# Kernel optimization log

Measured on AMD Instinct MI355X. Metric: run time of the kernel, lower is better.

## Reference

```python
import jax, jax.numpy as jnp
import numpy as np

M, N, K, C, G = 16384, 131072, 16, 128, 8
EPS_BN = 1e-5


def _bn(x, g, b):
    # inference-mode BatchNorm1d (running_mean=0, running_var=1)
    return x * (g / jnp.sqrt(1.0 + EPS_BN)) + b


def setup_inputs() -> dict:
    key = jax.random.key(0)
    ks = jax.random.split(key, 16)
    f32 = jnp.float32
    s = 0.05
    return {
        "query_feat": jax.random.normal(ks[0], (M, C), f32),
        "context_feat": jax.random.normal(ks[1], (N, C), f32),
        "query_coord": jax.random.normal(ks[2], (M, 3), f32),
        "context_coord": jax.random.normal(ks[3], (N, 3), f32),
        "Wq": jax.random.normal(ks[4], (C, C), f32) * s,
        "bq": jnp.zeros((C,), f32),
        "gq": jnp.ones((C,), f32),
        "betaq": jnp.zeros((C,), f32),
        "Wk": jax.random.normal(ks[5], (C, C), f32) * s,
        "bk": jnp.zeros((C,), f32),
        "gk": jnp.ones((C,), f32),
        "betak": jnp.zeros((C,), f32),
        "Wv": jax.random.normal(ks[6], (C, C), f32) * s,
        "bv": jnp.zeros((C,), f32),
        "Wp1": jax.random.normal(ks[7], (3, C), f32) * s,
        "bp1": jnp.zeros((C,), f32),
        "gp1": jnp.ones((C,), f32),
        "betap1": jnp.zeros((C,), f32),
        "Wp2": jax.random.normal(ks[8], (C, C), f32) * s,
        "bp2": jnp.zeros((C,), f32),
        "Ww1": jax.random.normal(ks[9], (C, G), f32) * s,
        "bw1": jnp.zeros((G,), f32),
        "gw1": jnp.ones((G,), f32),
        "betaw1": jnp.zeros((G,), f32),
        "Ww2": jax.random.normal(ks[10], (G, G), f32) * s,
        "bw2": jnp.zeros((G,), f32),
        "knn_indexes": jax.random.randint(ks[11], (M, K), 0, N, dtype=jnp.int32),
    }


def reference(query_feat, context_feat, query_coord, context_coord,
              Wq, bq, gq, betaq, Wk, bk, gk, betak, Wv, bv,
              Wp1, bp1, gp1, betap1, Wp2, bp2,
              Ww1, bw1, gw1, betaw1, Ww2, bw2, knn_indexes):
    q = jax.nn.relu(_bn(query_feat @ Wq + bq, gq, betaq))              # (M, C)
    k = jax.nn.relu(_bn(context_feat @ Wk + bk, gk, betak))            # (N, C)
    v = context_feat @ Wv + bv                                         # (N, C)

    mask = knn_indexes >= 0                                            # (M, K); -1 = padded neighbor
    idx = jnp.where(mask, knn_indexes, 0)
    mf = mask[..., None].astype(q.dtype)                               # (M, K, 1)

    key_g = k[idx] * mf                                                # (M, K, C) gather (zero row for -1)
    val_g = v[idx] * mf                                                # (M, K, C)
    pos = (context_coord[idx] - query_coord[:, None, :]) * mf          # (M, K, 3) relative position

    # positional-encoding bias branch (pe_bias=True, pe_multiplier=False)
    peb = jax.nn.relu(_bn(pos @ Wp1 + bp1, gp1, betap1)) @ Wp2 + bp2   # (M, K, C)
    rel = key_g - q[:, None, :] + peb                                  # (M, K, C)
    val_g = val_g + peb

    # grouped vector attention weights
    w = jax.nn.relu(_bn(rel @ Ww1 + bw1, gw1, betaw1)) @ Ww2 + bw2     # (M, K, G)
    w = jax.nn.softmax(w, axis=1) * mf                                 # softmax over neighbors, mask padded

    m_, k_ = idx.shape
    c_ = q.shape[-1]
    g_ = w.shape[-1]
    out = jnp.einsum('mkgi,mkg->mgi', val_g.reshape(m_, k_, g_, c_ // g_), w)
    return out.reshape(m_, c_)
```

## Files before the change

kernel.cpp:

```cpp
#include <hip/hip_runtime.h>

#define C 128
#define G 8
#define KNN 16
#define QB 4
#define EPS 1e-5f

typedef unsigned short u16;
typedef __attribute__((ext_vector_type(8))) short short8;
typedef __attribute__((ext_vector_type(4))) float float4v;

union frag_u { short8 v; u16 u[8]; unsigned d[4]; };

__device__ inline u16 f2bf(float f) {
    unsigned u = __builtin_bit_cast(unsigned, f);
    unsigned r = (u + 0x7fffu + ((u >> 16) & 1u)) >> 16;
    return (u16)r;
}
__device__ inline float bf2f(u16 h) {
    unsigned u = ((unsigned)h) << 16;
    return __builtin_bit_cast(float, u);
}
__device__ inline unsigned pk2(float lo, float hi) {
    unsigned r;
    asm("v_cvt_pk_bf16_f32 %0, %1, %2" : "=v"(r) : "v"(lo), "v"(hi));
    return r;
}
__device__ inline u16 f2bf1(float f) { return (u16)pk2(f, f); }
__device__ inline float bflo(unsigned v) { return __builtin_bit_cast(float, v << 16); }
__device__ inline float bfhi(unsigned v) { return __builtin_bit_cast(float, v & 0xffff0000u); }

__global__ __launch_bounds__(256) void prep_w(
    const float* __restrict__ Wk, const float* __restrict__ Wv,
    const float* __restrict__ Wq, const float* __restrict__ Wp2,
    const float* __restrict__ Ww1, const float* __restrict__ bp2,
    u16* __restrict__ dst, float* __restrict__ cw1)
{
    __shared__ float w1s[C * G];
    const int b = blockIdx.x, t = threadIdx.x;
    if (b < 16) {
        const int mi = b >> 2, qt = b & 3;
        const float* W = mi == 0 ? Wk : mi == 1 ? Wv : mi == 2 ? Wq : Wp2;
        u16* d = dst + mi * 16384;
        for (int e = qt * 4096 + t; e < (qt + 1) * 4096; e += 256) {
            const int k = e >> 7, n = e & 127;
            const int cb = n >> 4, lan = n & 15;
            const int kk = k >> 5, quad = (k >> 3) & 3, j = k & 7;
            d[(((cb * 4 + kk) * 4 + quad) * 16 + lan) * 8 + j] = f2bf(W[e]);
        }
    } else if (b == 16) {
        u16* d = dst + 4 * 16384;
        for (int e = t; e < 4096; e += 256) {
            const int j = e & 7, lan = (e >> 3) & 15;
            const int quad = (e >> 7) & 3, kk = e >> 9;
            const int k = kk * 32 + quad * 8 + j;
            d[e] = lan < 8 ? f2bf(Ww1[k * G + lan]) : (u16)0;
        }
    } else {
        u16* d = dst + 4 * 16384 + 4096;
        for (int e = t; e < 4096; e += 256) d[e] = 0;
        for (int e = t; e < C * G; e += 256) w1s[e] = Ww1[e];
        __syncthreads();
#pragma unroll
        for (int it = 0; it < 4; it++) {
            const int k = it * 32 + (t >> 3), g = t & 7;
            const float4* Wr = (const float4*)(Wp2 + k * C);
            float a = 0.f;
#pragma unroll 8
            for (int i4 = 0; i4 < 32; i4++) {
                const float4 wv = Wr[i4];
                a = fmaf(wv.x, w1s[(i4 * 4 + 0) * G + g], a);
                a = fmaf(wv.y, w1s[(i4 * 4 + 1) * G + g], a);
                a = fmaf(wv.z, w1s[(i4 * 4 + 2) * G + g], a);
                a = fmaf(wv.w, w1s[(i4 * 4 + 3) * G + g], a);
            }
            const int kk = k >> 5, quad = (k >> 3) & 3, j = k & 7;
            d[((kk * 4 + quad) * 16 + g) * 8 + j] = f2bf(a);
        }
        if (t < G) {
            float a = 0.f;
#pragma unroll 8
            for (int i = 0; i < C; i++) a = fmaf(bp2[i], w1s[i * G + t], a);
            cw1[t] = a;
        }
    }
}

__global__ __launch_bounds__(256) void proj_all(
    const float* __restrict__ Xc, const float* __restrict__ Xq,
    const u16* __restrict__ PWk, const float* __restrict__ bk,
    const float* __restrict__ gk, const float* __restrict__ betak,
    const u16* __restrict__ PWv, const float* __restrict__ bv,
    const u16* __restrict__ PWq, const float* __restrict__ bq,
    const float* __restrict__ gq, const float* __restrict__ betaq,
    const u16* __restrict__ PWw1b,
    u16* __restrict__ vout, u16* __restrict__ Kp, u16* __restrict__ Qp,
    int nkv)
{
    __shared__ u16 Xs[64 * 136];
    const int t = threadIdx.x;
    const int w = t >> 6, l = t & 63;
    const int quad = l >> 4, lan = l & 15;
    const bool isq = (int)blockIdx.x >= nkv;
    const long long row0 = (long long)(isq ? blockIdx.x - nkv : blockIdx.x) * 64;
    const float* X = isq ? Xq : Xc;

    {
        const float4* Xv = (const float4*)(X + row0 * C);
#pragma unroll
        for (int i = 0; i < 8; i++) {
            const int e = t + 256 * i;
            const int r = e >> 5, c4 = e & 31;
            const float4 f = Xv[e];
            uint2 p;
            p.x = pk2(f.x, f.y);
            p.y = pk2(f.z, f.w);
            *(uint2*)(&Xs[r * 136 + c4 * 4]) = p;
        }
    }
    __syncthreads();

    if (!isq) {
        unsigned vp[2][4][2];
        {
            short8 Bf[2][4];
#pragma unroll
            for (int ct = 0; ct < 2; ct++) {
                const int cb = w * 2 + ct;
#pragma unroll
                for (int kk = 0; kk < 4; kk++)
                    Bf[ct][kk] = *(const short8*)(PWv + (((cb * 4 + kk) * 4 + quad) * 16 + lan) * 8);
            }
            const float b0v = bv[w * 32 + lan], b1v = bv[w * 32 + 16 + lan];
            float4v acc[2][4];
#pragma unroll
            for (int rt = 0; rt < 4; rt++) {
                acc[0][rt] = (float4v)b0v;
                acc[1][rt] = (float4v)b1v;
            }
#pragma unroll
            for (int rt = 0; rt < 4; rt++)
#pragma unroll
                for (int kk = 0; kk < 4; kk++) {
                    const short8 A = *(const short8*)(&Xs[(rt * 16 + lan) * 136 + kk * 32 + quad * 8]);
#pragma unroll
                    for (int ct = 0; ct < 2; ct++)
                        acc[ct][rt] = __builtin_amdgcn_mfma_f32_16x16x32_bf16(
                            A, Bf[ct][kk], acc[ct][rt], 0, 0, 0);
                }
#pragma unroll
            for (int ct = 0; ct < 2; ct++)
#pragma unroll
                for (int rt = 0; rt < 4; rt++)
#pragma unroll
                    for (int h = 0; h < 2; h++)
                        vp[ct][rt][h] = pk2(acc[ct][rt][2 * h], acc[ct][rt][2 * h + 1]);
        }
        float4v acck[2][4];
        {
            short8 Bf[2][4];
#pragma unroll
            for (int ct = 0; ct < 2; ct++) {
                const int cb = w * 2 + ct;
#pragma unroll
                for (int kk = 0; kk < 4; kk++)
                    Bf[ct][kk] = *(const short8*)(PWk + (((cb * 4 + kk) * 4 + quad) * 16 + lan) * 8);
            }
            const float b0k = bk[w * 32 + lan], b1k = bk[w * 32 + 16 + lan];
#pragma unroll
            for (int rt = 0; rt < 4; rt++) {
                acck[0][rt] = (float4v)b0k;
                acck[1][rt] = (float4v)b1k;
            }
#pragma unroll
            for (int rt = 0; rt < 4; rt++)
#pragma unroll
                for (int kk = 0; kk < 4; kk++) {
                    const short8 A = *(const short8*)(&Xs[(rt * 16 + lan) * 136 + kk * 32 + quad * 8]);
#pragma unroll
                    for (int ct = 0; ct < 2; ct++)
                        acck[ct][rt] = __builtin_amdgcn_mfma_f32_16x16x32_bf16(
                            A, Bf[ct][kk], acck[ct][rt], 0, 0, 0);
                }
        }
        __syncthreads();

#pragma unroll
        for (int ct = 0; ct < 2; ct++) {
            const int cg = w * 32 + ct * 16 + lan;
            const float sc = gk[cg] * rsqrtf(1.f + EPS);
            const float sh = betak[cg];
#pragma unroll
            for (int rt = 0; rt < 4; rt++)
#pragma unroll
                for (int reg = 0; reg < 4; reg++) {
                    float y = fmaf(acck[ct][rt][reg], sc, sh);
                    y = y > 0.f ? y : 0.f;
                    Xs[(rt * 16 + quad * 4 + reg) * 136 + cg] = f2bf1(y);
                }
        }
        __syncthreads();

        {
            short8 Bw[4];
#pragma unroll
            for (int kk = 0; kk < 4; kk++)
                Bw[kk] = *(const short8*)(PWw1b + ((kk * 4 + quad) * 16 + lan) * 8);
            float4v ka = (float4v)0.f;
#pragma unroll
            for (int kk = 0; kk < 4; kk++) {
                const short8 A = *(const short8*)(&Xs[(w * 16 + lan) * 136 + kk * 32 + quad * 8]);
                ka = __builtin_amdgcn_mfma_f32_16x16x32_bf16(A, Bw[kk], ka, 0, 0, 0);
            }
            if (lan < G) {
#pragma unroll
                for (int reg = 0; reg < 4; reg++)
                    Kp[(row0 + w * 16 + quad * 4 + reg) * G + lan] = f2bf1(ka[reg]);
            }
        }
        __syncthreads();

#pragma unroll
        for (int ct = 0; ct < 2; ct++) {
            const int cg = w * 32 + ct * 16 + lan;
#pragma unroll
            for (int rt = 0; rt < 4; rt++)
#pragma unroll
                for (int h = 0; h < 2; h++) {
                    Xs[(rt * 16 + quad * 4 + 2 * h) * 136 + cg]     = (u16)(vp[ct][rt][h] & 0xffffu);
                    Xs[(rt * 16 + quad * 4 + 2 * h + 1) * 136 + cg] = (u16)(vp[ct][rt][h] >> 16);
                }
        }
        __syncthreads();
#pragma unroll
        for (int i = 0; i < 4; i++) {
            const int e = t + 256 * i;
            const int r = e >> 4, cc = (e & 15) * 8;
            *(short8*)(vout + (row0 + r) * C + cc) = *(const short8*)(&Xs[r * 136 + cc]);
        }
    } else {
        float4v acc[2][4];
        {
            short8 Bf[2][4];
#pragma unroll
            for (int ct = 0; ct < 2; ct++) {
                const int cb = w * 2 + ct;
#pragma unroll
                for (int kk = 0; kk < 4; kk++)
                    Bf[ct][kk] = *(const short8*)(PWq + (((cb * 4 + kk) * 4 + quad) * 16 + lan) * 8);
            }
            const float b0q = bq[w * 32 + lan], b1q = bq[w * 32 + 16 + lan];
#pragma unroll
            for (int rt = 0; rt < 4; rt++) {
                acc[0][rt] = (float4v)b0q;
                acc[1][rt] = (float4v)b1q;
            }
#pragma unroll
            for (int rt = 0; rt < 4; rt++)
#pragma unroll
                for (int kk = 0; kk < 4; kk++) {
                    const short8 A = *(const short8*)(&Xs[(rt * 16 + lan) * 136 + kk * 32 + quad * 8]);
#pragma unroll
                    for (int ct = 0; ct < 2; ct++)
                        acc[ct][rt] = __builtin_amdgcn_mfma_f32_16x16x32_bf16(
                            A, Bf[ct][kk], acc[ct][rt], 0, 0, 0);
                }
        }
        __syncthreads();
#pragma unroll
        for (int ct = 0; ct < 2; ct++) {
            const int cg = w * 32 + ct * 16 + lan;
            const float sc = gq[cg] * rsqrtf(1.f + EPS);
            const float sh = betaq[cg];
#pragma unroll
            for (int rt = 0; rt < 4; rt++)
#pragma unroll
                for (int reg = 0; reg < 4; reg++) {
                    float y = fmaf(acc[ct][rt][reg], sc, sh);
                    y = y > 0.f ? y : 0.f;
                    Xs[(rt * 16 + quad * 4 + reg) * 136 + cg] = f2bf1(y);
                }
        }
        __syncthreads();
        {
            short8 Bw[4];
#pragma unroll
            for (int kk = 0; kk < 4; kk++)
                Bw[kk] = *(const short8*)(PWw1b + ((kk * 4 + quad) * 16 + lan) * 8);
            float4v qa = (float4v)0.f;
#pragma unroll
            for (int kk = 0; kk < 4; kk++) {
                const short8 A = *(const short8*)(&Xs[(w * 16 + lan) * 136 + kk * 32 + quad * 8]);
                qa = __builtin_amdgcn_mfma_f32_16x16x32_bf16(A, Bw[kk], qa, 0, 0, 0);
            }
            if (lan < G) {
#pragma unroll
                for (int reg = 0; reg < 4; reg++)
                    Qp[(row0 + w * 16 + quad * 4 + reg) * G + lan] = f2bf1(qa[reg]);
            }
        }
    }
}

__global__ __launch_bounds__(256) void attn6(
    const u16* __restrict__ vbuf, const u16* __restrict__ Kp,
    const u16* __restrict__ Qp,
    const float* __restrict__ qcoord, const float* __restrict__ ccoord,
    const float* __restrict__ Wp1, const float* __restrict__ bp1,
    const float* __restrict__ gp1, const float* __restrict__ betap1,
    const u16* __restrict__ PWp2, const float* __restrict__ bp2,
    const u16* __restrict__ PWp2pb, const float* __restrict__ cw1,
    const float* __restrict__ bw1,
    const float* __restrict__ gw1, const float* __restrict__ betaw1,
    const float* __restrict__ Ww2, const float* __restrict__ bw2,
    const int* __restrict__ knn, float* __restrict__ out)
{
    __shared__ u16    fA[64 * 136];
    __shared__ u16    kgs[64 * G];
    __shared__ float  qps[QB * G];
    __shared__ float  pebp[64 * G];
    __shared__ float  cw1s[G];
    __shared__ float  ww2s[G * G];
    __shared__ float4 ps4[64];
    __shared__ int    idxs[64];
    __shared__ float  wl[QB * 16 * G];

    const int t = threadIdx.x;
    const int w = t >> 6, l = t & 63;
    const int quad = l >> 4, lan = l & 15;
    const int m0 = blockIdx.x * QB;
    const int rsub = t >> 4;
    const int c8 = (t & 15) * 8;

    float mfr[4];
    frag_u vg[4];
#pragma unroll
    for (int p = 0; p < 4; p++) {
        const int ii = knn[m0 * KNN + p * 16 + rsub];
        mfr[p] = ii >= 0 ? 1.f : 0.f;
        const size_t i0 = ii >= 0 ? ii : 0;
        vg[p].v = *(const short8*)(vbuf + i0 * C + c8);
    }
    if (t < 64) {
        const int q = t >> 4;
        const int ii = knn[m0 * KNN + t];
        const float mf = ii >= 0 ? 1.f : 0.f;
        const int i0 = ii >= 0 ? ii : 0;
        idxs[t] = ii;
        float4 p4;
        p4.x = (ccoord[i0 * 3 + 0] - qcoord[(m0 + q) * 3 + 0]) * mf;
        p4.y = (ccoord[i0 * 3 + 1] - qcoord[(m0 + q) * 3 + 1]) * mf;
        p4.z = (ccoord[i0 * 3 + 2] - qcoord[(m0 + q) * 3 + 2]) * mf;
        p4.w = 0.f;
        ps4[t] = p4;
        *(short8*)(&kgs[t * G]) = *(const short8*)(Kp + (size_t)i0 * G);
    } else if (t < 64 + QB) {
        const int p = t - 64;
        frag_u qv;
        qv.v = *(const short8*)(Qp + (size_t)(m0 + p) * G);
#pragma unroll
        for (int j = 0; j < G; j++) qps[p * G + j] = bf2f(qv.u[j]);
    } else if (t < 68 + G) {
        cw1s[t - 68] = cw1[t - 68];
    } else if (t < 76 + G * G) {
        ww2s[t - 76] = Ww2[t - 76];
    }
    __syncthreads();

    {
        const float rsq = rsqrtf(1.f + EPS);
        const float4 gA = *(const float4*)(&gp1[c8]);
        const float4 gB = *(const float4*)(&gp1[c8 + 4]);
        const float4 bA = *(const float4*)(&bp1[c8]);
        const float4 bB = *(const float4*)(&bp1[c8 + 4]);
        const float4 eA = *(const float4*)(&betap1[c8]);
        const float4 eB = *(const float4*)(&betap1[c8 + 4]);
        const float4 xA = *(const float4*)(&Wp1[c8]);
        const float4 xB = *(const float4*)(&Wp1[c8 + 4]);
        const float4 yA = *(const float4*)(&Wp1[C + c8]);
        const float4 yB = *(const float4*)(&Wp1[C + c8 + 4]);
        const float4 zA = *(const float4*)(&Wp1[2 * C + c8]);
        const float4 zB = *(const float4*)(&Wp1[2 * C + c8 + 4]);
        const float gs[8] = {gA.x, gA.y, gA.z, gA.w, gB.x, gB.y, gB.z, gB.w};
        const float bs[8] = {bA.x, bA.y, bA.z, bA.w, bB.x, bB.y, bB.z, bB.w};
        const float es[8] = {eA.x, eA.y, eA.z, eA.w, eB.x, eB.y, eB.z, eB.w};
        const float xs[8] = {xA.x, xA.y, xA.z, xA.w, xB.x, xB.y, xB.z, xB.w};
        const float ys[8] = {yA.x, yA.y, yA.z, yA.w, yB.x, yB.y, yB.z, yB.w};
        const float zs[8] = {zA.x, zA.y, zA.z, zA.w, zB.x, zB.y, zB.z, zB.w};
        float w0f[8], w1f[8], w2f[8], bbf[8];
#pragma unroll
        for (int i2 = 0; i2 < 8; i2++) {
            const float sc = gs[i2] * rsq;
            w0f[i2] = xs[i2] * sc;
            w1f[i2] = ys[i2] * sc;
            w2f[i2] = zs[i2] * sc;
            bbf[i2] = fmaf(bs[i2], sc, es[i2]);
        }
#pragma unroll
        for (int rr = 0; rr < 4; rr++) {
            const int r = rsub * 4 + rr;
            const float4 p4 = ps4[r];
            frag_u o;
#pragma unroll
            for (int dd = 0; dd < 4; dd++) {
                const int ca = 2 * dd, cb2 = 2 * dd + 1;
                float ya = fmaf(p4.x, w0f[ca],
                           fmaf(p4.y, w1f[ca], fmaf(p4.z, w2f[ca], bbf[ca])));
                float yb = fmaf(p4.x, w0f[cb2],
                           fmaf(p4.y, w1f[cb2], fmaf(p4.z, w2f[cb2], bbf[cb2])));
                ya = ya > 0.f ? ya : 0.f;
                yb = yb > 0.f ? yb : 0.f;
                o.d[dd] = pk2(ya, yb);
            }
            *(short8*)(&fA[r * 136 + c8]) = o.v;
        }
    }
    __syncthreads();

    float4v acc[2][4];
    float4v pp = (float4v)0.f;
    {
        short8 Bf[2][4];
#pragma unroll
        for (int ct = 0; ct < 2; ct++) {
            const int cb = w * 2 + ct;
#pragma unroll
            for (int kk = 0; kk < 4; kk++)
                Bf[ct][kk] = *(const short8*)(PWp2 + (((cb * 4 + kk) * 4 + quad) * 16 + lan) * 8);
        }
        const float b0 = bp2[w * 32 + lan], b1 = bp2[w * 32 + 16 + lan];
#pragma unroll
        for (int q = 0; q < 4; q++) {
            acc[0][q] = (float4v)b0;
            acc[1][q] = (float4v)b1;
        }
#pragma unroll
        for (int q = 0; q < 4; q++)
#pragma unroll
            for (int kk = 0; kk < 4; kk++) {
                const short8 A = *(const short8*)(&fA[(q * 16 + lan) * 136 + kk * 32 + quad * 8]);
#pragma unroll
                for (int ct = 0; ct < 2; ct++)
                    acc[ct][q] = __builtin_amdgcn_mfma_f32_16x16x32_bf16(
                        A, Bf[ct][kk], acc[ct][q], 0, 0, 0);
            }
#pragma unroll
        for (int kk = 0; kk < 4; kk++) {
            const short8 Bp = *(const short8*)(PWp2pb + ((kk * 4 + quad) * 16 + lan) * 8);
            const short8 A = *(const short8*)(&fA[(w * 16 + lan) * 136 + kk * 32 + quad * 8]);
            pp = __builtin_amdgcn_mfma_f32_16x16x32_bf16(A, Bp, pp, 0, 0, 0);
        }
    }
    __syncthreads();

    {
#pragma unroll
        for (int ct = 0; ct < 2; ct++)
#pragma unroll
            for (int q = 0; q < 4; q++)
#pragma unroll
                for (int reg = 0; reg < 4; reg++)
                    fA[(q * 16 + quad * 4 + reg) * 136 + w * 32 + ct * 16 + lan] =
                        f2bf1(acc[ct][q][reg]);
        if (lan < G) {
#pragma unroll
            for (int reg = 0; reg < 4; reg++)
                pebp[(w * 16 + quad * 4 + reg) * G + lan] = pp[reg];
        }
    }
    __syncthreads();

    {
#pragma unroll
        for (int p = 0; p < 4; p++) {
            const int r = p * 16 + rsub;
            const float mf = mfr[p];
            frag_u peb, o;
            peb.v = *(const short8*)(&fA[r * 136 + c8]);
#pragma unroll
            for (int dd = 0; dd < 4; dd++) {
                const unsigned pv = peb.d[dd], vv = vg[p].d[dd];
                o.d[dd] = pk2(fmaf(bflo(vv), mf, bflo(pv)),
                              fmaf(bfhi(vv), mf, bfhi(pv)));
            }
            *(short8*)(&fA[r * 136 + c8]) = o.v;
        }
    }
    {
        const int j = l & 15;
        const int r = (w << 4) + j;
        const float mf = idxs[r] >= 0 ? 1.f : 0.f;
        const int g0 = 2 * quad, g1 = g0 + 1;
        const float L0 = bf2f(kgs[r * G + g0]) * mf - qps[w * G + g0]
                       + pebp[r * G + g0] + cw1s[g0] + bw1[g0];
        const float L1 = bf2f(kgs[r * G + g1]) * mf - qps[w * G + g1]
                       + pebp[r * G + g1] + cw1s[g1] + bw1[g1];
        const float y0 = L0 * (gw1[g0] * rsqrtf(1.f + EPS)) + betaw1[g0];
        const float y1 = L1 * (gw1[g1] * rsqrtf(1.f + EPS)) + betaw1[g1];
        wl[w * 128 + j * 8 + g0] = y0 > 0.f ? y0 : 0.f;
        wl[w * 128 + j * 8 + g1] = y1 > 0.f ? y1 : 0.f;
    }
    __syncthreads();

    {
        const int j = l & 15;
        const int g0 = 2 * quad, g1 = g0 + 1;
        float hw_[8];
#pragma unroll
        for (int g = 0; g < 8; g++) hw_[g] = wl[w * 128 + j * 8 + g];
        float a0 = bw2[g0], a1 = bw2[g1];
#pragma unroll
        for (int g = 0; g < 8; g++) {
            a0 = fmaf(hw_[g], ww2s[g * 8 + g0], a0);
            a1 = fmaf(hw_[g], ww2s[g * 8 + g1], a1);
        }
        float mx0 = a0, mx1 = a1;
#pragma unroll
        for (int off = 1; off < 16; off <<= 1) {
            mx0 = fmaxf(mx0, __shfl_xor(mx0, off));
            mx1 = fmaxf(mx1, __shfl_xor(mx1, off));
        }
        const float e0 = __expf(a0 - mx0), e1 = __expf(a1 - mx1);
        float s0 = e0, s1 = e1;
#pragma unroll
        for (int off = 1; off < 16; off <<= 1) {
            s0 += __shfl_xor(s0, off);
            s1 += __shfl_xor(s1, off);
        }
        const float mf = idxs[(w << 4) + j] >= 0 ? 1.f : 0.f;
        wl[w * 128 + j * 8 + g0] = e0 * (1.f / s0) * mf;
        wl[w * 128 + j * 8 + g1] = e1 * (1.f / s1) * mf;
    }
    __syncthreads();

    {
        const int q = t >> 6;
        const int pc = t & 63;
        const int c0 = 2 * pc;
        const int g = pc >> 3;
        float s0 = 0.f, s1 = 0.f;
#pragma unroll
        for (int j = 0; j < KNN; j++) {
            const unsigned v = *(const unsigned*)(&fA[(q * 16 + j) * 136 + c0]);
            const float wv = wl[q * 128 + j * 8 + g];
            s0 = fmaf(bflo(v), wv, s0);
            s1 = fmaf(bfhi(v), wv, s1);
        }
        *(float2*)(&out[(size_t)(m0 + q) * C + c0]) = make_float2(s0, s1);
    }
}

extern "C" void kernel_launch(void* const* d_in, const int* in_sizes, int n_in,
                              void* d_out, int out_size, void* d_ws, size_t ws_size,
                              hipStream_t stream)
{
    const float* query_feat    = (const float*)d_in[0];
    const float* context_feat  = (const float*)d_in[1];
    const float* query_coord   = (const float*)d_in[2];
    const float* context_coord = (const float*)d_in[3];
    const float* Wq    = (const float*)d_in[4];
    const float* bq    = (const float*)d_in[5];
    const float* gq    = (const float*)d_in[6];
    const float* betaq = (const float*)d_in[7];
    const float* Wk    = (const float*)d_in[8];
    const float* bk    = (const float*)d_in[9];
    const float* gk    = (const float*)d_in[10];
    const float* betak = (const float*)d_in[11];
    const float* Wv    = (const float*)d_in[12];
    const float* bv    = (const float*)d_in[13];
    const float* Wp1   = (const float*)d_in[14];
    const float* bp1   = (const float*)d_in[15];
    const float* gp1   = (const float*)d_in[16];
    const float* betap1= (const float*)d_in[17];
    const float* Wp2   = (const float*)d_in[18];
    const float* bp2   = (const float*)d_in[19];
    const float* Ww1   = (const float*)d_in[20];
    const float* bw1   = (const float*)d_in[21];
    const float* gw1   = (const float*)d_in[22];
    const float* betaw1= (const float*)d_in[23];
    const float* Ww2   = (const float*)d_in[24];
    const float* bw2   = (const float*)d_in[25];
    const int*   knn   = (const int*)d_in[26];

    const int M = in_sizes[0] / C;
    const int N = in_sizes[1] / C;

    u16* vb = (u16*)d_ws;
    u16* Kp = vb + (size_t)N * C;
    u16* Qp = Kp + (size_t)N * G;
    u16* pw = Qp + (size_t)M * G;
    u16* pWk    = pw;
    u16* pWv    = pw + 16384;
    u16* pWq    = pw + 2 * 16384;
    u16* pWp2   = pw + 3 * 16384;
    u16* pWw1b  = pw + 4 * 16384;
    u16* pWp2pb = pw + 4 * 16384 + 4096;
    float* cw1  = (float*)(pw + 4 * 16384 + 2 * 4096);

    prep_w<<<18, 256, 0, stream>>>(Wk, Wv, Wq, Wp2, Ww1, bp2, pw, cw1);
    proj_all<<<N / 64 + M / 64, 256, 0, stream>>>(
        context_feat, query_feat,
        pWk, bk, gk, betak, pWv, bv,
        pWq, bq, gq, betaq, pWw1b,
        vb, Kp, Qp, N / 64);
    attn6<<<M / QB, 256, 0, stream>>>(vb, Kp, Qp, query_coord, context_coord,
                                      Wp1, bp1, gp1, betap1, pWp2, bp2,
                                      pWp2pb, cw1, bw1, gw1, betaw1, Ww2, bw2,
                                      knn, (float*)d_out);
}
```

Measured before the change: 206.4 us.

## Process two query groups per block and prefetch next group's value gathers

The attention kernel now handles two groups of four queries per block in a loop, halving the grid size. All knn indices, coordinates, K/Q slices for both groups are loaded up front, and the value-row gather for the next group is issued in the middle of the current group's softmax phase so its latency overlaps compute. This adds an extra barrier per iteration and more registers and shared memory, and it reduces the number of blocks available for latency hiding.

After: 213.1 us. 3.3% more time.

```diff
diff --git a/kernel.cpp b/kernel.cpp
--- a/kernel.cpp
+++ b/kernel.cpp
@@ -4,6 +4,7 @@
 #define G 8
 #define KNN 16
 #define QB 4
+#define GROUPS 2
 #define EPS 1e-5f
 
 typedef unsigned short u16;
@@ -316,50 +317,63 @@
     const int* __restrict__ knn, float* __restrict__ out)
 {
     __shared__ u16    fA[64 * 136];
-    __shared__ u16    kgs[64 * G];
-    __shared__ float  qps[QB * G];
+    __shared__ u16    kgs[GROUPS][64 * G];
+    __shared__ float  qps[GROUPS][QB * G];
     __shared__ float  pebp[64 * G];
     __shared__ float  cw1s[G];
     __shared__ float  ww2s[G * G];
-    __shared__ float4 ps4[64];
-    __shared__ int    idxs[64];
+    __shared__ float4 ps4[GROUPS][64];
+    __shared__ int    idxs[GROUPS][64];
     __shared__ float  wl[QB * 16 * G];
 
     const int t = threadIdx.x;
     const int w = t >> 6, l = t & 63;
     const int quad = l >> 4, lan = l & 15;
-    const int m0 = blockIdx.x * QB;
+    const int mbase = blockIdx.x * (QB * GROUPS);
     const int rsub = t >> 4;
     const int c8 = (t & 15) * 8;
 
+    int knnreg[GROUPS][4];
+#pragma unroll
+    for (int gg = 0; gg < GROUPS; gg++)
+#pragma unroll
+        for (int p = 0; p < 4; p++)
+            knnreg[gg][p] = knn[(mbase + gg * QB) * KNN + p * 16 + rsub];
+
     float mfr[4];
     frag_u vg[4];
 #pragma unroll
     for (int p = 0; p < 4; p++) {
-        const int ii = knn[m0 * KNN + p * 16 + rsub];
+        const int ii = knnreg[0][p];
         mfr[p] = ii >= 0 ? 1.f : 0.f;
         const size_t i0 = ii >= 0 ? ii : 0;
         vg[p].v = *(const short8*)(vbuf + i0 * C + c8);
     }
     if (t < 64) {
-        const int q = t >> 4;
-        const int ii = knn[m0 * KNN + t];
-        const float mf = ii >= 0 ? 1.f : 0.f;
-        const int i0 = ii >= 0 ? ii : 0;
-        idxs[t] = ii;
-        float4 p4;
-        p4.x = (ccoord[i0 * 3 + 0] - qcoord[(m0 + q) * 3 + 0]) * mf;
-        p4.y = (ccoord[i0 * 3 + 1] - qcoord[(m0 + q) * 3 + 1]) * mf;
-        p4.z = (ccoord[i0 * 3 + 2] - qcoord[(m0 + q) * 3 + 2]) * mf;
-        p4.w = 0.f;
-        ps4[t] = p4;
-        *(short8*)(&kgs[t * G]) = *(const short8*)(Kp + (size_t)i0 * G);
+#pragma unroll
+        for (int gg = 0; gg < GROUPS; gg++) {
+            const int q = t >> 4;
+            const int ii = knn[(mbase + gg * QB) * KNN + t];
+            const float mf = ii >= 0 ? 1.f : 0.f;
+            const int i0 = ii >= 0 ? ii : 0;
+            idxs[gg][t] = ii;
+            float4 p4;
+            p4.x = (ccoord[i0 * 3 + 0] - qcoord[(mbase + gg * QB + q) * 3 + 0]) * mf;
+            p4.y = (ccoord[i0 * 3 + 1] - qcoord[(mbase + gg * QB + q) * 3 + 1]) * mf;
+            p4.z = (ccoord[i0 * 3 + 2] - qcoord[(mbase + gg * QB + q) * 3 + 2]) * mf;
+            p4.w = 0.f;
+            ps4[gg][t] = p4;
+            *(short8*)(&kgs[gg][t * G]) = *(const short8*)(Kp + (size_t)i0 * G);
+        }
     } else if (t < 64 + QB) {
         const int p = t - 64;
-        frag_u qv;
-        qv.v = *(const short8*)(Qp + (size_t)(m0 + p) * G);
-#pragma unroll
-        for (int j = 0; j < G; j++) qps[p * G + j] = bf2f(qv.u[j]);
+#pragma unroll
+        for (int gg = 0; gg < GROUPS; gg++) {
+            frag_u qv;
+            qv.v = *(const short8*)(Qp + (size_t)(mbase + gg * QB + p) * G);
+#pragma unroll
+            for (int j = 0; j < G; j++) qps[gg][p * G + j] = bf2f(qv.u[j]);
+        }
     } else if (t < 68 + G) {
         cw1s[t - 68] = cw1[t - 68];
     } else if (t < 76 + G * G) {
@@ -367,186 +381,202 @@
     }
     __syncthreads();
 
-    {
-        const float rsq = rsqrtf(1.f + EPS);
-        const float4 gA = *(const float4*)(&gp1[c8]);
-        const float4 gB = *(const float4*)(&gp1[c8 + 4]);
-        const float4 bA = *(const float4*)(&bp1[c8]);
-        const float4 bB = *(const float4*)(&bp1[c8 + 4]);
-        const float4 eA = *(const float4*)(&betap1[c8]);
-        const float4 eB = *(const float4*)(&betap1[c8 + 4]);
-        const float4 xA = *(const float4*)(&Wp1[c8]);
-        const float4 xB = *(const float4*)(&Wp1[c8 + 4]);
-        const float4 yA = *(const float4*)(&Wp1[C + c8]);
-        const float4 yB = *(const float4*)(&Wp1[C + c8 + 4]);
-        const float4 zA = *(const float4*)(&Wp1[2 * C + c8]);
-        const float4 zB = *(const float4*)(&Wp1[2 * C + c8 + 4]);
-        const float gs[8] = {gA.x, gA.y, gA.z, gA.w, gB.x, gB.y, gB.z, gB.w};
-        const float bs[8] = {bA.x, bA.y, bA.z, bA.w, bB.x, bB.y, bB.z, bB.w};
-        const float es[8] = {eA.x, eA.y, eA.z, eA.w, eB.x, eB.y, eB.z, eB.w};
-        const float xs[8] = {xA.x, xA.y, xA.z, xA.w, xB.x, xB.y, xB.z, xB.w};
-        const float ys[8] = {yA.x, yA.y, yA.z, yA.w, yB.x, yB.y, yB.z, yB.w};
-        const float zs[8] = {zA.x, zA.y, zA.z, zA.w, zB.x, zB.y, zB.z, zB.w};
-        float w0f[8], w1f[8], w2f[8], bbf[8];
-#pragma unroll
-        for (int i2 = 0; i2 < 8; i2++) {
-            const float sc = gs[i2] * rsq;
-            w0f[i2] = xs[i2] * sc;
-            w1f[i2] = ys[i2] * sc;
-            w2f[i2] = zs[i2] * sc;
-            bbf[i2] = fmaf(bs[i2], sc, es[i2]);
-        }
-#pragma unroll
-        for (int rr = 0; rr < 4; rr++) {
-            const int r = rsub * 4 + rr;
-            const float4 p4 = ps4[r];
-            frag_u o;
-#pragma unroll
-            for (int dd = 0; dd < 4; dd++) {
-                const int ca = 2 * dd, cb2 = 2 * dd + 1;
-                float ya = fmaf(p4.x, w0f[ca],
-                           fmaf(p4.y, w1f[ca], fmaf(p4.z, w2f[ca], bbf[ca])));
-                float yb = fmaf(p4.x, w0f[cb2],
-                           fmaf(p4.y, w1f[cb2], fmaf(p4.z, w2f[cb2], bbf[cb2])));
-                ya = ya > 0.f ? ya : 0.f;
-                yb = yb > 0.f ? yb : 0.f;
-                o.d[dd] = pk2(ya, yb);
-            }
-            *(short8*)(&fA[r * 136 + c8]) = o.v;
-        }
-    }
-    __syncthreads();
-
-    float4v acc[2][4];
-    float4v pp = (float4v)0.f;
-    {
-        short8 Bf[2][4];
-#pragma unroll
-        for (int ct = 0; ct < 2; ct++) {
-            const int cb = w * 2 + ct;
-#pragma unroll
-            for (int kk = 0; kk < 4; kk++)
-                Bf[ct][kk] = *(const short8*)(PWp2 + (((cb * 4 + kk) * 4 + quad) * 16 + lan) * 8);
-        }
-        const float b0 = bp2[w * 32 + lan], b1 = bp2[w * 32 + 16 + lan];
-#pragma unroll
-        for (int q = 0; q < 4; q++) {
-            acc[0][q] = (float4v)b0;
-            acc[1][q] = (float4v)b1;
-        }
-#pragma unroll
-        for (int q = 0; q < 4; q++)
+#pragma unroll
+    for (int gi = 0; gi < GROUPS; gi++) {
+        const int m0 = mbase + gi * QB;
+
+        {
+            const float rsq = rsqrtf(1.f + EPS);
+            const float4 gA = *(const float4*)(&gp1[c8]);
+            const float4 gB = *(const float4*)(&gp1[c8 + 4]);
+            const float4 bA = *(const float4*)(&bp1[c8]);
+            const float4 bB = *(const float4*)(&bp1[c8 + 4]);
+            const float4 eA = *(const float4*)(&betap1[c8]);
+            const float4 eB = *(const float4*)(&betap1[c8 + 4]);
+            const float4 xA = *(const float4*)(&Wp1[c8]);
+            const float4 xB = *(const float4*)(&Wp1[c8 + 4]);
+            const float4 yA = *(const float4*)(&Wp1[C + c8]);
+            const float4 yB = *(const float4*)(&Wp1[C + c8 + 4]);
+            const float4 zA = *(const float4*)(&Wp1[2 * C + c8]);
+            const float4 zB = *(const float4*)(&Wp1[2 * C + c8 + 4]);
+            const float gs[8] = {gA.x, gA.y, gA.z, gA.w, gB.x, gB.y, gB.z, gB.w};
+            const float bs[8] = {bA.x, bA.y, bA.z, bA.w, bB.x, bB.y, bB.z, bB.w};
+            const float es[8] = {eA.x, eA.y, eA.z, eA.w, eB.x, eB.y, eB.z, eB.w};
+            const float xs[8] = {xA.x, xA.y, xA.z, xA.w, xB.x, xB.y, xB.z, xB.w};
+            const float ys[8] = {yA.x, yA.y, yA.z, yA.w, yB.x, yB.y, yB.z, yB.w};
+            const float zs[8] = {zA.x, zA.y, zA.z, zA.w, zB.x, zB.y, zB.z, zB.w};
+            float w0f[8], w1f[8], w2f[8], bbf[8];
+#pragma unroll
+            for (int i2 = 0; i2 < 8; i2++) {
+                const float sc = gs[i2] * rsq;
+                w0f[i2] = xs[i2] * sc;
+                w1f[i2] = ys[i2] * sc;
+                w2f[i2] = zs[i2] * sc;
+                bbf[i2] = fmaf(bs[i2], sc, es[i2]);
+            }
+#pragma unroll
+            for (int rr = 0; rr < 4; rr++) {
+                const int r = rsub * 4 + rr;
+                const float4 p4 = ps4[gi][r];
+                frag_u o;
+#pragma unroll
+                for (int dd = 0; dd < 4; dd++) {
+                    const int ca = 2 * dd, cb2 = 2 * dd + 1;
+                    float ya = fmaf(p4.x, w0f[ca],
+                               fmaf(p4.y, w1f[ca], fmaf(p4.z, w2f[ca], bbf[ca])));
+                    float yb = fmaf(p4.x, w0f[cb2],
+                               fmaf(p4.y, w1f[cb2], fmaf(p4.z, w2f[cb2], bbf[cb2])));
+                    ya = ya > 0.f ? ya : 0.f;
+                    yb = yb > 0.f ? yb : 0.f;
+                    o.d[dd] = pk2(ya, yb);
+                }
+                *(short8*)(&fA[r * 136 + c8]) = o.v;
+            }
+        }
+        __syncthreads();
+
+        float4v acc[2][4];
+        float4v pp = (float4v)0.f;
+        {
+            short8 Bf[2][4];
+#pragma unroll
+            for (int ct = 0; ct < 2; ct++) {
+                const int cb = w * 2 + ct;
+#pragma unroll
+                for (int kk = 0; kk < 4; kk++)
+                    Bf[ct][kk] = *(const short8*)(PWp2 + (((cb * 4 + kk) * 4 + quad) * 16 + lan) * 8);
+            }
+            const float b0 = bp2[w * 32 + lan], b1 = bp2[w * 32 + 16 + lan];
+#pragma unroll
+            for (int q = 0; q < 4; q++) {
+                acc[0][q] = (float4v)b0;
+                acc[1][q] = (float4v)b1;
+            }
+#pragma unroll
+            for (int q = 0; q < 4; q++)
+#pragma unroll
+                for (int kk = 0; kk < 4; kk++) {
+                    const short8 A = *(const short8*)(&fA[(q * 16 + lan) * 136 + kk * 32 + quad * 8]);
+#pragma unroll
+                    for (int ct = 0; ct < 2; ct++)
+                        acc[ct][q] = __builtin_amdgcn_mfma_f32_16x16x32_bf16(
+                            A, Bf[ct][kk], acc[ct][q], 0, 0, 0);
+                }
 #pragma unroll
             for (int kk = 0; kk < 4; kk++) {
-                const short8 A = *(const short8*)(&fA[(q * 16 + lan) * 136 + kk * 32 + quad * 8]);
-#pragma unroll
-                for (int ct = 0; ct < 2; ct++)
-                    acc[ct][q] = __builtin_amdgcn_mfma_f32_16x16x32_bf16(
-                        A, Bf[ct][kk], acc[ct][q], 0, 0, 0);
-            }
-#pragma unroll
-        for (int kk = 0; kk < 4; kk++) {
-            const short8 Bp = *(const short8*)(PWp2pb + ((kk * 4 + quad) * 16 + lan) * 8);
-            const short8 A = *(const short8*)(&fA[(w * 16 + lan) * 136 + kk * 32 + quad * 8]);
-            pp = __builtin_amdgcn_mfma_f32_16x16x32_bf16(A, Bp, pp, 0, 0, 0);
-        }
-    }
-    __syncthreads();
-
-    {
-#pragma unroll
-        for (int ct = 0; ct < 2; ct++)
-#pragma unroll
-            for (int q = 0; q < 4; q++)
+                const short8 Bp = *(const short8*)(PWp2pb + ((kk * 4 + quad) * 16 + lan) * 8);
+                const short8 A = *(const short8*)(&fA[(w * 16 + lan) * 136 + kk * 32 + quad * 8]);
+                pp = __builtin_amdgcn_mfma_f32_16x16x32_bf16(A, Bp, pp, 0, 0, 0);
+            }
+        }
+        __syncthreads();
+
+        {
+#pragma unroll
+            for (int ct = 0; ct < 2; ct++)
+#pragma unroll
+                for (int q = 0; q < 4; q++)
+#pragma unroll
+                    for (int reg = 0; reg < 4; reg++)
+                        fA[(q * 16 + quad * 4 + reg) * 136 + w * 32 + ct * 16 + lan] =
+                            f2bf1(acc[ct][q][reg]);
+            if (lan < G) {
 #pragma unroll
                 for (int reg = 0; reg < 4; reg++)
-                    fA[(q * 16 + quad * 4 + reg) * 136 + w * 32 + ct * 16 + lan] =
-                        f2bf1(acc[ct][q][reg]);
-        if (lan < G) {
-#pragma unroll
-            for (int reg = 0; reg < 4; reg++)
-                pebp[(w * 16 + quad * 4 + reg) * G + lan] = pp[reg];
-        }
-    }
-    __syncthreads();
-
-    {
-#pragma unroll
-        for (int p = 0; p < 4; p++) {
-            const int r = p * 16 + rsub;
-            const float mf = mfr[p];
-            frag_u peb, o;
-            peb.v = *(const short8*)(&fA[r * 136 + c8]);
-#pragma unroll
-            for (int dd = 0; dd < 4; dd++) {
-                const unsigned pv = peb.d[dd], vv = vg[p].d[dd];
-                o.d[dd] = pk2(fmaf(bflo(vv), mf, bflo(pv)),
-                              fmaf(bfhi(vv), mf, bfhi(pv)));
-            }
-            *(short8*)(&fA[r * 136 + c8]) = o.v;
-        }
-    }
-    {
-        const int j = l & 15;
-        const int r = (w << 4) + j;
-        const float mf = idxs[r] >= 0 ? 1.f : 0.f;
-        const int g0 = 2 * quad, g1 = g0 + 1;
-        const float L0 = bf2f(kgs[r * G + g0]) * mf - qps[w * G + g0]
-                       + pebp[r * G + g0] + cw1s[g0] + bw1[g0];
-        const float L1 = bf2f(kgs[r * G + g1]) * mf - qps[w * G + g1]
-                       + pebp[r * G + g1] + cw1s[g1] + bw1[g1];
-        const float y0 = L0 * (gw1[g0] * rsqrtf(1.f + EPS)) + betaw1[g0];
-        const float y1 = L1 * (gw1[g1] * rsqrtf(1.f + EPS)) + betaw1[g1];
-        wl[w * 128 + j * 8 + g0] = y0 > 0.f ? y0 : 0.f;
-        wl[w * 128 + j * 8 + g1] = y1 > 0.f ? y1 : 0.f;
-    }
-    __syncthreads();
-
-    {
-        const int j = l & 15;
-        const int g0 = 2 * quad, g1 = g0 + 1;
-        float hw_[8];
-#pragma unroll
-        for (int g = 0; g < 8; g++) hw_[g] = wl[w * 128 + j * 8 + g];
-        float a0 = bw2[g0], a1 = bw2[g1];
-#pragma unroll
-        for (int g = 0; g < 8; g++) {
-            a0 = fmaf(hw_[g], ww2s[g * 8 + g0], a0);
-            a1 = fmaf(hw_[g], ww2s[g * 8 + g1], a1);
-        }
-        float mx0 = a0, mx1 = a1;
-#pragma unroll
-        for (int off = 1; off < 16; off <<= 1) {
-            mx0 = fmaxf(mx0, __shfl_xor(mx0, off));
-            mx1 = fmaxf(mx1, __shfl_xor(mx1, off));
-        }
-        const float e0 = __expf(a0 - mx0), e1 = __expf(a1 - mx1);
-        float s0 = e0, s1 = e1;
-#pragma unroll
-        for (int off = 1; off < 16; off <<= 1) {
-            s0 += __shfl_xor(s0, off);
-            s1 += __shfl_xor(s1, off);
-        }
-        const float mf = idxs[(w << 4) + j] >= 0 ? 1.f : 0.f;
-        wl[w * 128 + j * 8 + g0] = e0 * (1.f / s0) * mf;
-        wl[w * 128 + j * 8 + g1] = e1 * (1.f / s1) * mf;
-    }
-    __syncthreads();
-
-    {
-        const int q = t >> 6;
-        const int pc = t & 63;
-        const int c0 = 2 * pc;
-        const int g = pc >> 3;
-        float s0 = 0.f, s1 = 0.f;
-#pragma unroll
-        for (int j = 0; j < KNN; j++) {
-            const unsigned v = *(const unsigned*)(&fA[(q * 16 + j) * 136 + c0]);
-            const float wv = wl[q * 128 + j * 8 + g];
-            s0 = fmaf(bflo(v), wv, s0);
-            s1 = fmaf(bfhi(v), wv, s1);
-        }
-        *(float2*)(&out[(size_t)(m0 + q) * C + c0]) = make_float2(s0, s1);
+                    pebp[(w * 16 + quad * 4 + reg) * G + lan] = pp[reg];
+            }
+        }
+        __syncthreads();
+
+        {
+#pragma unroll
+            for (int p = 0; p < 4; p++) {
+                const int r = p * 16 + rsub;
+                const float mf = mfr[p];
+                frag_u peb, o;
+                peb.v = *(const short8*)(&fA[r * 136 + c8]);
+#pragma unroll
+                for (int dd = 0; dd < 4; dd++) {
+                    const unsigned pv = peb.d[dd], vv = vg[p].d[dd];
+                    o.d[dd] = pk2(fmaf(bflo(vv), mf, bflo(pv)),
+                                  fmaf(bfhi(vv), mf, bfhi(pv)));
+                }
+                *(short8*)(&fA[r * 136 + c8]) = o.v;
+            }
+        }
+        if (gi + 1 < GROUPS) {
+#pragma unroll
+            for (int p = 0; p < 4; p++) {
+                const int ii = knnreg[gi + 1][p];
+                mfr[p] = ii >= 0 ? 1.f : 0.f;
+                const size_t i0 = ii >= 0 ? ii : 0;
+                vg[p].v = *(const short8*)(vbuf + i0 * C + c8);
+            }
+        }
+        {
+            const int j = l & 15;
+            const int r = (w << 4) + j;
+            const float mf = idxs[gi][r] >= 0 ? 1.f : 0.f;
+            const int g0 = 2 * quad, g1 = g0 + 1;
+            const float L0 = bf2f(kgs[gi][r * G + g0]) * mf - qps[gi][w * G + g0]
+                           + pebp[r * G + g0] + cw1s[g0] + bw1[g0];
+            const float L1 = bf2f(kgs[gi][r * G + g1]) * mf - qps[gi][w * G + g1]
+                           + pebp[r * G + g1] + cw1s[g1] + bw1[g1];
+            const float y0 = L0 * (gw1[g0] * rsqrtf(1.f + EPS)) + betaw1[g0];
+            const float y1 = L1 * (gw1[g1] * rsqrtf(1.f + EPS)) + betaw1[g1];
+            wl[w * 128 + j * 8 + g0] = y0 > 0.f ? y0 : 0.f;
+            wl[w * 128 + j * 8 + g1] = y1 > 0.f ? y1 : 0.f;
+        }
+        __syncthreads();
+
+        {
+            const int j = l & 15;
+            const int g0 = 2 * quad, g1 = g0 + 1;
+            float hw_[8];
+#pragma unroll
+            for (int g = 0; g < 8; g++) hw_[g] = wl[w * 128 + j * 8 + g];
+            float a0 = bw2[g0], a1 = bw2[g1];
+#pragma unroll
+            for (int g = 0; g < 8; g++) {
+                a0 = fmaf(hw_[g], ww2s[g * 8 + g0], a0);
+                a1 = fmaf(hw_[g], ww2s[g * 8 + g1], a1);
+            }
+            float mx0 = a0, mx1 = a1;
+#pragma unroll
+            for (int off = 1; off < 16; off <<= 1) {
+                mx0 = fmaxf(mx0, __shfl_xor(mx0, off));
+                mx1 = fmaxf(mx1, __shfl_xor(mx1, off));
+            }
+            const float e0 = __expf(a0 - mx0), e1 = __expf(a1 - mx1);
+            float s0 = e0, s1 = e1;
+#pragma unroll
+            for (int off = 1; off < 16; off <<= 1) {
+                s0 += __shfl_xor(s0, off);
+                s1 += __shfl_xor(s1, off);
+            }
+            const float mf = idxs[gi][(w << 4) + j] >= 0 ? 1.f : 0.f;
+            wl[w * 128 + j * 8 + g0] = e0 * (1.f / s0) * mf;
+            wl[w * 128 + j * 8 + g1] = e1 * (1.f / s1) * mf;
+        }
+        __syncthreads();
+
+        {
+            const int q = t >> 6;
+            const int pc = t & 63;
+            const int c0 = 2 * pc;
+            const int g = pc >> 3;
+            float s0 = 0.f, s1 = 0.f;
+#pragma unroll
+            for (int j = 0; j < KNN; j++) {
+                const unsigned v = *(const unsigned*)(&fA[(q * 16 + j) * 136 + c0]);
+                const float wv = wl[q * 128 + j * 8 + g];
+                s0 = fmaf(bflo(v), wv, s0);
+                s1 = fmaf(bfhi(v), wv, s1);
+            }
+            *(float2*)(&out[(size_t)(m0 + q) * C + c0]) = make_float2(s0, s1);
+        }
+
+        if (gi + 1 < GROUPS) __syncthreads();
     }
 }
 
@@ -603,8 +633,9 @@
         pWk, bk, gk, betak, pWv, bv,
         pWq, bq, gq, betaq, pWw1b,
         vb, Kp, Qp, N / 64);
-    attn6<<<M / QB, 256, 0, stream>>>(vb, Kp, Qp, query_coord, context_coord,
-                                      Wp1, bp1, gp1, betap1, pWp2, bp2,
-                                      pWp2pb, cw1, bw1, gw1, betaw1, Ww2, bw2,
-                                      knn, (float*)d_out);
+    attn6<<<M / (QB * GROUPS), 256, 0, stream>>>(
+        vb, Kp, Qp, query_coord, context_coord,
+        Wp1, bp1, gp1, betap1, pWp2, bp2,
+        pWp2pb, cw1, bw1, gw1, betaw1, Ww2, bw2,
+        knn, (float*)d_out);
 }
```
